# Performance work log

Hardware: AMD Instinct MI355X
Metric: run time of the kernel (lower is better)

The kernel has to match this reference:

```python
import jax, jax.numpy as jnp
from jax import lax
import numpy as np

B, S, D_IN, D_H, D_OUT, FUTURE = 64, 512, 1024, 2048, 1024, 16


def setup_inputs() -> dict:
    key = jax.random.key(0)
    k1, k2, k3 = jax.random.split(key, 3)
    x = jax.random.normal(k1, (B, S, D_IN), dtype=jnp.float32)
    # nn.Linear(input+hidden -> hidden): y = z @ Wh + bh (Wh stores W^T layout)
    Wh = jax.random.normal(k2, (D_IN + D_H, D_H), dtype=jnp.float32) * 0.02
    bh = jnp.zeros((D_H,), dtype=jnp.float32)
    Wo = jax.random.normal(k3, (D_H, D_OUT), dtype=jnp.float32) * 0.02
    bo = jnp.zeros((D_OUT,), dtype=jnp.float32)
    return {"x": x, "Wh": Wh, "bh": bh, "Wo": Wo, "bo": bo, "future": FUTURE}


def reference(x, Wh, bh, Wo, bo, future):
    batch, seq_len, _ = x.shape
    hidden_dim = Wh.shape[1]

    def cell(h, inp):
        # concat + linear + tanh, exactly RnnCell.forward
        combined = jnp.concatenate([inp, h], axis=1)  # [B, D_in + D_h]
        return jnp.tanh(combined @ Wh + bh)

    def step(h, xt):
        h = cell(h, xt)
        return h, h @ Wo + bo

    h0 = jnp.zeros((batch, hidden_dim), dtype=x.dtype)
    # scan over time: xs shaped [S, B, D_in]
    h_last, outs = lax.scan(step, h0, jnp.swapaxes(x, 0, 1))
    output = jnp.swapaxes(outs, 0, 1)  # [B, S, D_out]

    def fstep(carry, _):
        h, inp = carry
        h = cell(h, inp)
        out = h @ Wo + bo
        return (h, out), out  # feed output back as next input

    if future > 0:
        _, pouts = lax.scan(fstep, (h_last, x[:, -1, :]), None, length=future)
        predict = jnp.swapaxes(pouts, 0, 1)  # [B, future, D_out]
    else:
        predict = jnp.zeros((batch, 0, Wo.shape[1]), dtype=x.dtype)
    return output, predict
```

## Files before the change

### kernel.cpp

```cpp
#include <hip/hip_runtime.h>
#include <hip/hip_bf16.h>
#include <math.h>

#define Bz   64
#define Sz   512
#define DIN  1024
#define DH   2048
#define DOUT 1024
#define FUT  16
#define KTOT (DIN + DH)

typedef __attribute__((ext_vector_type(8))) __bf16 bf16x8;
typedef __attribute__((ext_vector_type(4))) float  f32x4;

union U16x8 { uint4 u; bf16x8 v; };

__device__ __forceinline__ uint4 pack_bf8(float4 a, float4 b) {
  bf16x8 t;
  t[0]=(__bf16)a.x; t[1]=(__bf16)a.y; t[2]=(__bf16)a.z; t[3]=(__bf16)a.w;
  t[4]=(__bf16)b.x; t[5]=(__bf16)b.y; t[6]=(__bf16)b.z; t[7]=(__bf16)b.w;
  U16x8 u; u.v = t; return u.u;
}

__device__ __forceinline__ float fast_tanh(float x) {
  const float e = __builtin_amdgcn_exp2f(2.8853900817779268f * x);
  return 1.0f - 2.0f * __builtin_amdgcn_rcpf(e + 1.0f);
}

template<bool AF32>
__device__ __forceinline__ void gemm_core(
    const void* __restrict__ Abase, size_t astride,
    const __bf16* __restrict__ Bbase, size_t bstride,
    int K, f32x4 acc[2][2])
{
  __shared__ uint4 Al[2][512];
  __shared__ uint4 Bl[2][512];

  const int tid  = threadIdx.x;
  const int lane = tid & 63;
  const int wave = tid >> 6;
  const int wm = (wave >> 1) << 5;
  const int wn = (wave & 1) << 5;
  const int fr = lane & 15;
  const int fg = lane >> 4;

  const int srow = tid >> 2;
  const int sck  = (tid & 3) << 1;

  const int NK = K >> 6;
  if (NK <= 0) return;

  uint4 ra0, ra1, rb0, rb1;

  auto loadt = [&](int kt) {
    const int kelt = (kt << 6) + (sck << 3);
    if constexpr (AF32) {
      const float* ap = (const float*)Abase + (size_t)srow * astride + kelt;
      float4 a0 = *(const float4*)(ap);
      float4 a1 = *(const float4*)(ap + 4);
      float4 a2 = *(const float4*)(ap + 8);
      float4 a3 = *(const float4*)(ap + 12);
      ra0 = pack_bf8(a0, a1);
      ra1 = pack_bf8(a2, a3);
    } else {
      const __bf16* ap = (const __bf16*)Abase + (size_t)srow * astride + kelt;
      ra0 = *(const uint4*)(ap);
      ra1 = *(const uint4*)(ap + 8);
    }
    const __bf16* bp = Bbase + (size_t)srow * bstride + kelt;
    rb0 = *(const uint4*)(bp);
    rb1 = *(const uint4*)(bp + 8);
  };

  auto storet = [&](int buf) {
    const int x7 = srow & 7;
    Al[buf][srow * 8 + ( sck      ^ x7)] = ra0;
    Al[buf][srow * 8 + ((sck + 1) ^ x7)] = ra1;
    Bl[buf][srow * 8 + ( sck      ^ x7)] = rb0;
    Bl[buf][srow * 8 + ((sck + 1) ^ x7)] = rb1;
  };

  loadt(0);
  storet(0);
  __syncthreads();

  for (int kt = 0; kt < NK; ++kt) {
    const int  cur  = kt & 1;
    const bool more = (kt + 1) < NK;
    if (more) loadt(kt + 1);

    #pragma unroll
    for (int kk = 0; kk < 2; ++kk) {
      bf16x8 af[2], bfrag[2];
      #pragma unroll
      for (int mi = 0; mi < 2; ++mi) {
        const int row = wm + mi * 16 + fr;
        const int ck  = (kk * 4 + fg) ^ (row & 7);
        U16x8 u; u.u = Al[cur][row * 8 + ck]; af[mi] = u.v;
      }
      #pragma unroll
      for (int ni = 0; ni < 2; ++ni) {
        const int row = wn + ni * 16 + fr;
        const int ck  = (kk * 4 + fg) ^ (row & 7);
        U16x8 u; u.u = Bl[cur][row * 8 + ck]; bfrag[ni] = u.v;
      }
      #pragma unroll
      for (int mi = 0; mi < 2; ++mi)
        #pragma unroll
        for (int ni = 0; ni < 2; ++ni)
          acc[mi][ni] = __builtin_amdgcn_mfma_f32_16x16x32_bf16(
              af[mi], bfrag[ni], acc[mi][ni], 0, 0, 0);
    }

    __syncthreads();
    if (more) storet((kt + 1) & 1);
    __syncthreads();
  }
}

#define EPI_SETUP() \
  const int tid = threadIdx.x, lane = tid & 63, wave = tid >> 6; \
  const int wm = (wave >> 1) << 5, wn = (wave & 1) << 5; \
  const int fr = lane & 15, fg = lane >> 4;

__global__ __launch_bounds__(256) void k_transp(const float* __restrict__ W,
                                                __bf16* __restrict__ WT,
                                                int K, int N)
{
  __shared__ float T[64][65];
  const int k0 = blockIdx.x << 6, n0 = blockIdx.y << 6;
  const int c = threadIdx.x & 63, r4 = threadIdx.x >> 6;
  #pragma unroll
  for (int rr = 0; rr < 16; ++rr) {
    const int r = rr * 4 + r4;
    T[r][c] = W[(size_t)(k0 + r) * N + n0 + c];
  }
  __syncthreads();
  #pragma unroll
  for (int rr = 0; rr < 16; ++rr) {
    const int r = rr * 4 + r4;
    WT[(size_t)(n0 + r) * K + k0 + c] = (__bf16)T[c][r];
  }
}

__global__ __launch_bounds__(256) void k_gemm_xw(const float* __restrict__ x,
                                                 const __bf16* __restrict__ WhT,
                                                 const float* __restrict__ bh,
                                                 __bf16* __restrict__ HX)
{
  const int s = blockIdx.x;
  const int n0 = blockIdx.y << 6;
  f32x4 acc[2][2] = {};
  gemm_core<true>(x + (size_t)s * DIN, (size_t)Sz * DIN,
                  WhT + (size_t)n0 * KTOT, KTOT, DIN, acc);
  EPI_SETUP();
  __bf16* out = HX + (size_t)s * Bz * DH;
  #pragma unroll
  for (int mi = 0; mi < 2; ++mi)
    #pragma unroll
    for (int ni = 0; ni < 2; ++ni)
      #pragma unroll
      for (int r = 0; r < 4; ++r) {
        const int m = wm + mi * 16 + fg * 4 + r;
        const int n = n0 + wn + ni * 16 + fr;
        out[(size_t)m * DH + n] = (__bf16)(acc[mi][ni][r] + bh[n]);
      }
}

__global__ __launch_bounds__(512, 2) void k_rnn(const __bf16* __restrict__ WhT,
                                                __bf16* __restrict__ HX,
                                                unsigned int* __restrict__ flags)
{
  __shared__ __align__(16) float RED[8 * 1056];

  const int mb    = blockIdx.x & 3;
  const int nb    = blockIdx.x >> 2;
  const int nbase = nb << 6;
  const int tid   = threadIdx.x;
  const int lane  = tid & 63;
  const int w     = tid >> 6;
  const int l15   = lane & 15;
  const int l4    = lane >> 4;
  const int wavek = w << 8;

  bf16x8 wf[8][4];
  {
    const __bf16* wb = WhT + (size_t)(nbase + l15) * KTOT + DIN + wavek + (l4 << 3);
    #pragma unroll
    for (int kk = 0; kk < 8; ++kk)
      #pragma unroll
      for (int nt = 0; nt < 4; ++nt)
        wf[kk][nt] = *(const bf16x8*)(wb + (size_t)nt * 16 * KTOT + kk * 32);
  }

  const int orow = tid >> 5;
  const int cp   = tid & 31;
  const int grow = (mb << 4) + orow;
  const int gcol = nbase + (cp << 1);

  for (int t = 0; t < Sz; ++t) {
    __bf16* Hc = HX + (size_t)t * Bz * DH;

    unsigned int xwp;
    asm volatile("global_load_dword %0, %1, off sc0 sc1"
                 : "=v"(xwp)
                 : "v"((const void*)(Hc + (size_t)grow * DH + gcol))
                 : "memory");

    f32x4 acc[4] = {};

    if (t > 0) {
      const unsigned int* fl = flags
          + (((size_t)(t - 1) * 4 + mb) << 7) + (((w << 2) + (lane & 3)) << 2);
      for (;;) {
        unsigned int f;
        asm volatile("global_load_dword %0, %1, off sc0 sc1\n\t"
                     "s_waitcnt vmcnt(0)"
                     : "=v"(f) : "v"((const void*)fl) : "memory");
        if (__all((int)(f == 1u))) break;
        __builtin_amdgcn_s_sleep(1);
      }

      const __bf16* Hp = HX + (size_t)(t - 1) * Bz * DH
                       + (size_t)((mb << 4) + l15) * DH + wavek + (l4 << 3);
      bf16x8 a[8];
      #pragma unroll
      for (int kk = 0; kk < 8; ++kk)
        a[kk] = *(const bf16x8*)(Hp + kk * 32);

      #pragma unroll
      for (int kk = 0; kk < 8; ++kk)
        #pragma unroll
        for (int nt = 0; nt < 4; ++nt)
          acc[nt] = __builtin_amdgcn_mfma_f32_16x16x32_bf16(
              a[kk], wf[kk][nt], acc[nt], 0, 0, 0);
    }

    #pragma unroll
    for (int nt = 0; nt < 4; ++nt)
      #pragma unroll
      for (int r = 0; r < 4; ++r)
        RED[w * 1056 + ((l4 << 2) + r) * 66 + (nt << 4) + l15] = acc[nt][r];
    __syncthreads();

    float sx = 0.f, sy = 0.f;
    #pragma unroll
    for (int p = 0; p < 8; ++p) {
      const float2 v = *(const float2*)&RED[p * 1056 + orow * 66 + (cp << 1)];
      sx += v.x; sy += v.y;
    }

    asm volatile("s_waitcnt vmcnt(0)" : "+v"(xwp) :: "memory");
    union { unsigned int u; __bf16 h[2]; } ux; ux.u = xwp;
    union { unsigned int u; __bf16 h[2]; } po;
    po.h[0] = (__bf16)fast_tanh(sx + (float)ux.h[0]);
    po.h[1] = (__bf16)fast_tanh(sy + (float)ux.h[1]);

    asm volatile("global_store_dword %0, %1, off sc0 sc1"
                 :: "v"((void*)(Hc + (size_t)grow * DH + gcol)), "v"(po.u)
                 : "memory");
    asm volatile("s_waitcnt vmcnt(0)" ::: "memory");
    __syncthreads();
    if (tid == 0) {
      unsigned int* fp = flags + (((size_t)t * 4 + mb) << 7) + (nb << 2);
      asm volatile("global_store_dword %0, %1, off sc0 sc1"
                   :: "v"((void*)fp), "v"(1u) : "memory");
    }
  }
}

__global__ __launch_bounds__(256) void k_out(const __bf16* __restrict__ HX,
                                             const __bf16* __restrict__ WoT,
                                             const float* __restrict__ bo,
                                             float* __restrict__ out)
{
  const int s = blockIdx.x;
  const int n0 = blockIdx.y << 6;
  f32x4 acc[2][2] = {};
  gemm_core<false>(HX + (size_t)s * Bz * DH, DH,
                   WoT + (size_t)n0 * DH, DH, DH, acc);
  EPI_SETUP();
  #pragma unroll
  for (int mi = 0; mi < 2; ++mi)
    #pragma unroll
    for (int ni = 0; ni < 2; ++ni)
      #pragma unroll
      for (int r = 0; r < 4; ++r) {
        const int m = wm + mi * 16 + fg * 4 + r;
        const int n = n0 + wn + ni * 16 + fr;
        out[((size_t)m * Sz + s) * DOUT + n] = acc[mi][ni][r] + bo[n];
      }
}

__global__ __launch_bounds__(256) void k_finit(const float* __restrict__ x,
                                               const __bf16* __restrict__ HX,
                                               __bf16* __restrict__ zf0)
{
  const int b = blockIdx.x;
  for (int k = threadIdx.x; k < DIN; k += 256)
    zf0[(size_t)b * KTOT + k] =
        (__bf16)x[((size_t)b * Sz + (Sz - 1)) * DIN + k];
  for (int k = threadIdx.x; k < DH; k += 256)
    zf0[(size_t)b * KTOT + DIN + k] =
        HX[(size_t)(Sz - 1) * Bz * DH + (size_t)b * DH + k];
}

__global__ __launch_bounds__(256) void k_fstep(const __bf16* __restrict__ zc,
                                               __bf16* __restrict__ zn,
                                               const __bf16* __restrict__ WhT,
                                               const float* __restrict__ bh)
{
  const int n0 = blockIdx.x << 6;
  f32x4 acc[2][2] = {};
  gemm_core<false>(zc, KTOT, WhT + (size_t)n0 * KTOT, KTOT, KTOT, acc);
  EPI_SETUP();
  #pragma unroll
  for (int mi = 0; mi < 2; ++mi)
    #pragma unroll
    for (int ni = 0; ni < 2; ++ni)
      #pragma unroll
      for (int r = 0; r < 4; ++r) {
        const int m = wm + mi * 16 + fg * 4 + r;
        const int n = n0 + wn + ni * 16 + fr;
        zn[(size_t)m * KTOT + DIN + n] = (__bf16)fast_tanh(acc[mi][ni][r] + bh[n]);
      }
}

__global__ __launch_bounds__(256) void k_fout(__bf16* __restrict__ zn,
                                              const __bf16* __restrict__ WoT,
                                              const float* __restrict__ bo,
                                              float* __restrict__ pred,
                                              int f)
{
  const int n0 = blockIdx.x << 6;
  f32x4 acc[2][2] = {};
  gemm_core<false>(zn + DIN, KTOT, WoT + (size_t)n0 * DH, DH, DH, acc);
  EPI_SETUP();
  #pragma unroll
  for (int mi = 0; mi < 2; ++mi)
    #pragma unroll
    for (int ni = 0; ni < 2; ++ni)
      #pragma unroll
      for (int r = 0; r < 4; ++r) {
        const int m = wm + mi * 16 + fg * 4 + r;
        const int n = n0 + wn + ni * 16 + fr;
        const float v = acc[mi][ni][r] + bo[n];
        pred[((size_t)m * FUT + f) * DOUT + n] = v;
        zn[(size_t)m * KTOT + n] = (__bf16)v;
      }
}

extern "C" void kernel_launch(void* const* d_in, const int* in_sizes, int n_in,
                              void* d_out, int out_size, void* d_ws, size_t ws_size,
                              hipStream_t stream)
{
  const float* x  = (const float*)d_in[0];
  const float* Wh = (const float*)d_in[1];
  const float* bh = (const float*)d_in[2];
  const float* Wo = (const float*)d_in[3];
  const float* bo = (const float*)d_in[4];

  char* ws = (char*)d_ws;
  __bf16* WhT = (__bf16*)ws;
  __bf16* WoT = WhT + (size_t)DH * KTOT;
  __bf16* HX  = WoT + (size_t)DOUT * DH;
  __bf16* zf  = HX + (size_t)Sz * Bz * DH;
  unsigned int* flags = (unsigned int*)(zf + (size_t)2 * Bz * KTOT);

  float* out  = (float*)d_out;
  float* pred = out + (size_t)Bz * Sz * DOUT;

  const dim3 blk(256);

  k_transp<<<dim3(KTOT / 64, DH / 64), blk, 0, stream>>>(Wh, WhT, KTOT, DH);
  k_transp<<<dim3(DH / 64, DOUT / 64), blk, 0, stream>>>(Wo, WoT, DH, DOUT);

  hipMemsetAsync(flags, 0, (size_t)Sz * 4 * 128 * sizeof(unsigned int), stream);

  k_gemm_xw<<<dim3(Sz, DH / 64), blk, 0, stream>>>(x, WhT, bh, HX);

  {
    const __bf16* a0 = WhT; __bf16* a1 = HX; unsigned int* a2 = flags;
    void* args[] = { (void*)&a0, (void*)&a1, (void*)&a2 };
    hipLaunchCooperativeKernel((const void*)k_rnn, dim3(128), dim3(512), args,
                               0, stream);
  }

  k_out<<<dim3(Sz, DOUT / 64), blk, 0, stream>>>(HX, WoT, bo, out);

  k_finit<<<dim3(Bz), blk, 0, stream>>>(x, HX, zf);
  for (int f = 0; f < FUT; ++f) {
    __bf16* zc = zf + (size_t)(f & 1) * Bz * KTOT;
    __bf16* zn = zf + (size_t)((f & 1) ^ 1) * Bz * KTOT;
    k_fstep<<<dim3(DH / 64), blk, 0, stream>>>(zc, zn, WhT, bh);
    k_fout<<<dim3(DOUT / 64), blk, 0, stream>>>(zn, WoT, bo, pred, f);
  }
}
```

Baseline: 3.572 ms.

## Replace input and output projection GEMMs with 128x128 tiled LDS-DMA kernels

Swaps the 64x64-tile GEMMs for the input projection and the output projection for new 128x128-tile kernels. The new kernels load tiles straight into LDS with global_load_lds, use an XOR swizzle to avoid bank conflicts, and run a 4x4 MFMA fragment grid per wave for more operand reuse. The aim is to cut global traffic and raise MFMA utilisation in the two large batched GEMMs. The recurrent kernel's MFMA is also switched to inline asm that takes its weight operand from AGPRs, which is meant to reduce register pressure and copies.

```diff
diff --git a/kernel.cpp b/kernel.cpp
--- a/kernel.cpp
+++ b/kernel.cpp
@@ -25,6 +25,12 @@
 __device__ __forceinline__ float fast_tanh(float x) {
   const float e = __builtin_amdgcn_exp2f(2.8853900817779268f * x);
   return 1.0f - 2.0f * __builtin_amdgcn_rcpf(e + 1.0f);
+}
+
+__device__ __forceinline__ void gload16(const void* g, void* l) {
+  __builtin_amdgcn_global_load_lds(
+      (const __attribute__((address_space(1))) unsigned int*)g,
+      (__attribute__((address_space(3))) unsigned int*)l, 16, 0, 0);
 }
 
 template<bool AF32>
@@ -143,28 +149,144 @@
   }
 }
 
-__global__ __launch_bounds__(256) void k_gemm_xw(const float* __restrict__ x,
-                                                 const __bf16* __restrict__ WhT,
-                                                 const float* __restrict__ bh,
-                                                 __bf16* __restrict__ HX)
-{
-  const int s = blockIdx.x;
-  const int n0 = blockIdx.y << 6;
-  f32x4 acc[2][2] = {};
-  gemm_core<true>(x + (size_t)s * DIN, (size_t)Sz * DIN,
-                  WhT + (size_t)n0 * KTOT, KTOT, DIN, acc);
-  EPI_SETUP();
-  __bf16* out = HX + (size_t)s * Bz * DH;
-  #pragma unroll
-  for (int mi = 0; mi < 2; ++mi)
-    #pragma unroll
-    for (int ni = 0; ni < 2; ++ni)
-      #pragma unroll
-      for (int r = 0; r < 4; ++r) {
-        const int m = wm + mi * 16 + fg * 4 + r;
-        const int n = n0 + wn + ni * 16 + fr;
-        out[(size_t)m * DH + n] = (__bf16)(acc[mi][ni][r] + bh[n]);
-      }
+__global__ __launch_bounds__(256) void k_xw128(const float* __restrict__ x,
+                                               const __bf16* __restrict__ WhT,
+                                               const float* __restrict__ bh,
+                                               __bf16* __restrict__ HX)
+{
+  __shared__ __align__(16) uint4 As[1024];
+  __shared__ __align__(16) uint4 Bs[1024];
+
+  const int n0 = blockIdx.x << 7;
+  const int m0 = blockIdx.y << 7;
+  const int tid = threadIdx.x, lane = tid & 63, w = tid >> 6;
+  const int wr = w >> 1, wc = w & 1;
+  const int fr = lane & 15, fg = lane >> 4;
+
+  const int sr  = tid >> 3;
+  const int sq  = tid & 7;
+  const int sq2 = sq ^ (sr & 7);
+
+  f32x4 acc[4][4] = {};
+
+  for (int kt = 0; kt < DIN / 64; ++kt) {
+    const int ko = kt << 6;
+    #pragma unroll
+    for (int j = 0; j < 4; ++j) {
+      const float* ap = x + (size_t)(m0 + sr + 32 * j) * DIN + ko + (sq2 << 3);
+      float4 a0 = *(const float4*)ap;
+      float4 a1 = *(const float4*)(ap + 4);
+      As[((sr + 32 * j) << 3) + sq] = pack_bf8(a0, a1);
+      gload16(WhT + (size_t)(n0 + sr + 32 * j) * KTOT + ko + (sq2 << 3),
+              (char*)Bs + (tid << 4) + (j << 12));
+    }
+    __syncthreads();
+    #pragma unroll
+    for (int kk = 0; kk < 2; ++kk) {
+      bf16x8 af[4], bf_[4];
+      const int kq = (kk << 2) + fg;
+      #pragma unroll
+      for (int mi = 0; mi < 4; ++mi) {
+        const int row = (wr << 6) + (mi << 4) + fr;
+        U16x8 u; u.u = As[(row << 3) + (kq ^ (row & 7))]; af[mi] = u.v;
+      }
+      #pragma unroll
+      for (int ni = 0; ni < 4; ++ni) {
+        const int row = (wc << 6) + (ni << 4) + fr;
+        U16x8 u; u.u = Bs[(row << 3) + (kq ^ (row & 7))]; bf_[ni] = u.v;
+      }
+      #pragma unroll
+      for (int mi = 0; mi < 4; ++mi)
+        #pragma unroll
+        for (int ni = 0; ni < 4; ++ni)
+          acc[mi][ni] = __builtin_amdgcn_mfma_f32_16x16x32_bf16(
+              af[mi], bf_[ni], acc[mi][ni], 0, 0, 0);
+    }
+    __syncthreads();
+  }
+
+  #pragma unroll
+  for (int ni = 0; ni < 4; ++ni) {
+    const int n = n0 + (wc << 6) + (ni << 4) + fr;
+    const float bn = bh[n];
+    #pragma unroll
+    for (int mi = 0; mi < 4; ++mi)
+      #pragma unroll
+      for (int rr = 0; rr < 4; ++rr) {
+        const int gf = m0 + (wr << 6) + (mi << 4) + (fg << 2) + rr;
+        const int b = gf >> 9, s = gf & 511;
+        HX[((size_t)s * Bz + b) * DH + n] = (__bf16)(acc[mi][ni][rr] + bn);
+      }
+  }
+}
+
+__global__ __launch_bounds__(256) void k_out128(const __bf16* __restrict__ HX,
+                                                const __bf16* __restrict__ WoT,
+                                                const float* __restrict__ bo,
+                                                float* __restrict__ out)
+{
+  __shared__ __align__(16) uint4 As[1024];
+  __shared__ __align__(16) uint4 Bs[1024];
+
+  const int n0 = blockIdx.x << 7;
+  const int m0 = blockIdx.y << 7;
+  const int tid = threadIdx.x, lane = tid & 63, w = tid >> 6;
+  const int wr = w >> 1, wc = w & 1;
+  const int fr = lane & 15, fg = lane >> 4;
+
+  const int sr  = tid >> 3;
+  const int sq  = tid & 7;
+  const int sq2 = sq ^ (sr & 7);
+
+  f32x4 acc[4][4] = {};
+
+  for (int kt = 0; kt < DH / 64; ++kt) {
+    const int ko = kt << 6;
+    #pragma unroll
+    for (int j = 0; j < 4; ++j) {
+      gload16(HX + (size_t)(m0 + sr + 32 * j) * DH + ko + (sq2 << 3),
+              (char*)As + (tid << 4) + (j << 12));
+      gload16(WoT + (size_t)(n0 + sr + 32 * j) * DH + ko + (sq2 << 3),
+              (char*)Bs + (tid << 4) + (j << 12));
+    }
+    __syncthreads();
+    #pragma unroll
+    for (int kk = 0; kk < 2; ++kk) {
+      bf16x8 af[4], bf_[4];
+      const int kq = (kk << 2) + fg;
+      #pragma unroll
+      for (int mi = 0; mi < 4; ++mi) {
+        const int row = (wr << 6) + (mi << 4) + fr;
+        U16x8 u; u.u = As[(row << 3) + (kq ^ (row & 7))]; af[mi] = u.v;
+      }
+      #pragma unroll
+      for (int ni = 0; ni < 4; ++ni) {
+        const int row = (wc << 6) + (ni << 4) + fr;
+        U16x8 u; u.u = Bs[(row << 3) + (kq ^ (row & 7))]; bf_[ni] = u.v;
+      }
+      #pragma unroll
+      for (int mi = 0; mi < 4; ++mi)
+        #pragma unroll
+        for (int ni = 0; ni < 4; ++ni)
+          acc[mi][ni] = __builtin_amdgcn_mfma_f32_16x16x32_bf16(
+              af[mi], bf_[ni], acc[mi][ni], 0, 0, 0);
+    }
+    __syncthreads();
+  }
+
+  #pragma unroll
+  for (int ni = 0; ni < 4; ++ni) {
+    const int n = n0 + (wc << 6) + (ni << 4) + fr;
+    const float bn = bo[n];
+    #pragma unroll
+    for (int mi = 0; mi < 4; ++mi)
+      #pragma unroll
+      for (int rr = 0; rr < 4; ++rr) {
+        const int gf = m0 + (wr << 6) + (mi << 4) + (fg << 2) + rr;
+        const int s = gf >> 6, b = gf & 63;
+        out[((size_t)b * Sz + s) * DOUT + n] = acc[mi][ni][rr] + bn;
+      }
+  }
 }
 
 __global__ __launch_bounds__(512, 2) void k_rnn(const __bf16* __restrict__ WhT,
@@ -232,8 +354,8 @@
       for (int kk = 0; kk < 8; ++kk)
         #pragma unroll
         for (int nt = 0; nt < 4; ++nt)
-          acc[nt] = __builtin_amdgcn_mfma_f32_16x16x32_bf16(
-              a[kk], wf[kk][nt], acc[nt], 0, 0, 0);
+          asm("v_mfma_f32_16x16x32_bf16 %0, %1, %2, %0"
+              : "+v"(acc[nt]) : "v"(a[kk]), "a"(wf[kk][nt]));
     }
 
     #pragma unroll
@@ -267,29 +389,6 @@
                    :: "v"((void*)fp), "v"(1u) : "memory");
     }
   }
-}
-
-__global__ __launch_bounds__(256) void k_out(const __bf16* __restrict__ HX,
-                                             const __bf16* __restrict__ WoT,
-                                             const float* __restrict__ bo,
-                                             float* __restrict__ out)
-{
-  const int s = blockIdx.x;
-  const int n0 = blockIdx.y << 6;
-  f32x4 acc[2][2] = {};
-  gemm_core<false>(HX + (size_t)s * Bz * DH, DH,
-                   WoT + (size_t)n0 * DH, DH, DH, acc);
-  EPI_SETUP();
-  #pragma unroll
-  for (int mi = 0; mi < 2; ++mi)
-    #pragma unroll
-    for (int ni = 0; ni < 2; ++ni)
-      #pragma unroll
-      for (int r = 0; r < 4; ++r) {
-        const int m = wm + mi * 16 + fg * 4 + r;
-        const int n = n0 + wn + ni * 16 + fr;
-        out[((size_t)m * Sz + s) * DOUT + n] = acc[mi][ni][r] + bo[n];
-      }
 }
 
 __global__ __launch_bounds__(256) void k_finit(const float* __restrict__ x,
@@ -377,7 +476,7 @@
 
   hipMemsetAsync(flags, 0, (size_t)Sz * 4 * 128 * sizeof(unsigned int), stream);
 
-  k_gemm_xw<<<dim3(Sz, DH / 64), blk, 0, stream>>>(x, WhT, bh, HX);
+  k_xw128<<<dim3(DH / 128, (Bz * Sz) / 128), blk, 0, stream>>>(x, WhT, bh, HX);
 
   {
     const __bf16* a0 = WhT; __bf16* a1 = HX; unsigned int* a2 = flags;
@@ -386,7 +485,7 @@
                                0, stream);
   }
 
-  k_out<<<dim3(Sz, DOUT / 64), blk, 0, stream>>>(HX, WoT, bo, out);
+  k_out128<<<dim3(DOUT / 128, (Bz * Sz) / 128), blk, 0, stream>>>(HX, WoT, bo, out);
 
   k_finit<<<dim3(Bz), blk, 0, stream>>>(x, HX, zf);
   for (int f = 0; f < FUT; ++f) {
```

Result: faster. 3.216 ms (median of 3 runs) (-10.0%).
